# Optimization experiments

Measured on AMD Instinct MI355X. Metric: run time of the kernel, lower is better.

The kernel has to match this reference:

```python
import math
import jax, jax.numpy as jnp
import numpy as np

B, NQ, NKV, D, H = 32, 512, 512, 1024, 8
DH = D // H              # 128
N_COLS = 512             # n + 1
D_COL = math.ceil(2 * math.log2(N_COLS))  # 18


def setup_inputs() -> dict:
    key = jax.random.key(0)
    ks = jax.random.split(key, 8)
    s = 0.02
    return {
        "x_q": jax.random.normal(ks[0], (B, NQ, D), jnp.float32),
        "x_kv": jax.random.normal(ks[1], (B, NKV, D), jnp.float32),
        # sym_weight=True => W_tail is W_head (shared)
        "W_head_w": jax.random.normal(ks[2], (D, D), jnp.float32) * s,
        "W_head_b": jnp.zeros((D,), jnp.float32),
        "W_v_w": jax.random.normal(ks[3], (D, D), jnp.float32) * s,
        "W_v_b": jnp.zeros((D,), jnp.float32),
        "W_out_w": jax.random.normal(ks[4], (D, D), jnp.float32) * s,
        "W_out_b": jnp.zeros((D,), jnp.float32),
        "rel_emb": jnp.ones((H, DH), jnp.float32),
        "col_head": jax.random.normal(ks[5], (H, N_COLS, D_COL), jnp.float32) * 0.2,
        "col_tail": jax.random.normal(ks[6], (H, N_COLS, D_COL), jnp.float32) * 0.2,
    }


def _heads(x, W, b, h, dh):
    # Linear then split heads: [B, n, d] -> [B, H, n, dh]
    B_, n, _ = x.shape
    y = x @ W.T + b
    return y.reshape(B_, n, h, dh).transpose(0, 2, 1, 3)


def reference(x_q, x_kv, W_head_w, W_head_b, W_v_w, W_v_b,
              W_out_w, W_out_b, rel_emb, col_head, col_tail):
    Bb, nq, d = x_q.shape
    nkv = x_kv.shape[1]
    h, dh = rel_emb.shape

    f_head = _heads(x_q, W_head_w, W_head_b, h, dh) * rel_emb[None, :, None, :]
    f_tail = _heads(x_kv, W_head_w, W_head_b, h, dh) * rel_emb[None, :, None, :]  # W_tail = W_head (sym_weight)
    f_v = _heads(x_kv, W_v_w, W_v_b, h, dh)

    # content score: [B, H, nq, nkv]
    weight_score = jnp.einsum('bhqd,bhkd->bhqk', f_head, f_tail) / math.sqrt(dh)

    # learned column topology: [H, n_cols, n_cols]
    adj_logits = jnp.einsum('hqc,hkc->hqk', col_head, col_tail)
    eye = jnp.eye(adj_logits.shape[-1], dtype=bool)  # nsi: zero diagonal before softmax
    adj_logits = jnp.where(eye[None], 0.0, adj_logits)
    adj = jax.nn.softmax(adj_logits, axis=-1)[:, :nq, :nkv]

    adj_mask = (1.0 - adj) * -10000.0
    fr_graph = jax.nn.softmax(weight_score + adj_mask[None], axis=-1)

    x = jnp.einsum('bhqk,bhkd->bhqd', fr_graph, f_v)
    x = x.transpose(0, 2, 1, 3).reshape(Bb, nq, h * dh)
    x = x @ W_out_w.T + W_out_b
    return (x, fr_graph.reshape(Bb * h, nq, nkv))
```

## Files before the change

### kernel.cpp

```cpp
#include <hip/hip_runtime.h>

typedef __attribute__((ext_vector_type(8))) __bf16 bf8;
typedef __attribute__((ext_vector_type(4))) __bf16 bf4;
typedef __attribute__((ext_vector_type(4))) float f32x4;

#define DEVI static __device__ __forceinline__

DEVI void gload_lds16(const void* g, void* l) {
  __builtin_amdgcn_global_load_lds(
      (const __attribute__((address_space(1))) unsigned int*)g,
      (__attribute__((address_space(3))) unsigned int*)l, 16, 0, 0);
}

__global__ __launch_bounds__(256) void cvt_kernel(const float* __restrict__ in,
                                                  __bf16* __restrict__ out, int n4) {
  int stride = gridDim.x * blockDim.x;
  for (int i = blockIdx.x * blockDim.x + threadIdx.x; i < n4; i += stride) {
    f32x4 v = reinterpret_cast<const f32x4*>(in)[i];
    bf4 o;
    o[0] = (__bf16)v[0]; o[1] = (__bf16)v[1]; o[2] = (__bf16)v[2]; o[3] = (__bf16)v[3];
    reinterpret_cast<bf4*>(out)[i] = o;
  }
}

template <int MODE>
__global__ __launch_bounds__(256) void gemm_proj(
    const __bf16* __restrict__ A, const __bf16* __restrict__ Bw,
    const float* __restrict__ bias, const float* __restrict__ rel,
    __bf16* __restrict__ obf, float* __restrict__ of32) {
  __shared__ alignas(16) __bf16 As[128 * 64];
  __shared__ alignas(16) __bf16 Bs[128 * 64];
  const int tid = threadIdx.x;
  const int lane = tid & 63;
  const int wave = tid >> 6;
  const int wr = wave >> 1, wc = wave & 1;
  const int lr = lane & 15, lk = (lane >> 4) * 8;

  f32x4 acc[4][4];
#pragma unroll
  for (int i = 0; i < 4; ++i)
#pragma unroll
    for (int j = 0; j < 4; ++j)
#pragma unroll
      for (int e = 0; e < 4; ++e) acc[i][j][e] = 0.f;

  const __bf16* Ab = A + (size_t)blockIdx.y * 128 * 1024;
  const __bf16* Bb = Bw + (size_t)blockIdx.x * 128 * 1024;
  const int sr = tid >> 3;
  const int sc = (tid & 7) * 8;

  for (int kt = 0; kt < 1024; kt += 64) {
#pragma unroll
    for (int i = 0; i < 4; ++i) {
      gload_lds16(Ab + (size_t)(sr + i * 32) * 1024 + kt + sc, As + tid * 8 + i * 2048);
      gload_lds16(Bb + (size_t)(sr + i * 32) * 1024 + kt + sc, Bs + tid * 8 + i * 2048);
    }
    __syncthreads();
#pragma unroll
    for (int kk = 0; kk < 64; kk += 32) {
      bf8 a[4], b[4];
#pragma unroll
      for (int mi = 0; mi < 4; ++mi)
        a[mi] = *reinterpret_cast<const bf8*>(&As[(wr * 64 + mi * 16 + lr) * 64 + kk + lk]);
#pragma unroll
      for (int ni = 0; ni < 4; ++ni)
        b[ni] = *reinterpret_cast<const bf8*>(&Bs[(wc * 64 + ni * 16 + lr) * 64 + kk + lk]);
#pragma unroll
      for (int mi = 0; mi < 4; ++mi)
#pragma unroll
        for (int ni = 0; ni < 4; ++ni)
          acc[mi][ni] = __builtin_amdgcn_mfma_f32_16x16x32_bf16(a[mi], b[ni], acc[mi][ni], 0, 0, 0);
    }
    __syncthreads();
  }

  const int mBase = blockIdx.y * 128 + wr * 64;
  const int nBase = blockIdx.x * 128 + wc * 64;
#pragma unroll
  for (int mi = 0; mi < 4; ++mi) {
#pragma unroll
    for (int ni = 0; ni < 4; ++ni) {
      const int n = nBase + ni * 16 + lr;
#pragma unroll
      for (int r = 0; r < 4; ++r) {
        const int m = mBase + mi * 16 + (lane >> 4) * 4 + r;
        float v = acc[mi][ni][r] + bias[n];
        if (MODE == 0) v *= rel[n];
        if (MODE == 2) {
          of32[(size_t)m * 1024 + n] = v;
        } else if (MODE == 0) {
          size_t idx = ((size_t)((m >> 9) * 8 + (n >> 7))) * 65536 +
                       (size_t)(m & 511) * 128 + (n & 127);
          obf[idx] = (__bf16)v;
        } else {
          size_t idx = ((size_t)((m >> 9) * 8 + (n >> 7))) * 65536 +
                       (size_t)(n & 127) * 512 + (m & 511);
          obf[idx] = (__bf16)v;
        }
      }
    }
  }
}

__global__ __launch_bounds__(256) void adj_kernel(const float* __restrict__ ch_all,
                                                  const float* __restrict__ ct_all,
                                                  float* __restrict__ adjs) {
  const int wave = threadIdx.x >> 6, lane = threadIdx.x & 63;
  const int row = blockIdx.x * 4 + wave;
  const int h = row >> 9, i = row & 511;
  float ch[18];
  const float* chp = ch_all + ((size_t)h * 512 + i) * 18;
#pragma unroll
  for (int t = 0; t < 18; ++t) ch[t] = chp[t];
  float e[8];
  float m = -1e30f;
#pragma unroll
  for (int jj = 0; jj < 8; ++jj) {
    const int j = jj * 64 + lane;
    const float* ctp = ct_all + ((size_t)h * 512 + j) * 18;
    float d = 0.f;
#pragma unroll
    for (int t = 0; t < 18; ++t) d += ch[t] * ctp[t];
    if (j == i) d = 0.f;
    e[jj] = d;
    m = fmaxf(m, d);
  }
#pragma unroll
  for (int off = 32; off >= 1; off >>= 1) m = fmaxf(m, __shfl_xor(m, off));
  float s = 0.f;
#pragma unroll
  for (int jj = 0; jj < 8; ++jj) { e[jj] = __expf(e[jj] - m); s += e[jj]; }
#pragma unroll
  for (int off = 32; off >= 1; off >>= 1) s += __shfl_xor(s, off);
  const float inv = 10000.f / s;
  float* op = adjs + (size_t)h * 262144 + (size_t)i * 512;
#pragma unroll
  for (int jj = 0; jj < 8; ++jj) op[jj * 64 + lane] = e[jj] * inv;
}

__global__ __launch_bounds__(256) void fused_attn_kernel(
    const __bf16* __restrict__ fh, const __bf16* __restrict__ ft,
    const __bf16* __restrict__ fvT, const float* __restrict__ adjs,
    float* fr, __bf16* __restrict__ ctx) {
  __shared__ alignas(16) __bf16 Bt[128 * 128];
  const int tid = threadIdx.x;
  const int l = tid & 63, w = tid >> 6;
  const int qt = blockIdx.x;
  const int bh = blockIdx.y;
  const int b = bh >> 3, h = bh & 7;
  const int wrow = qt * 64 + w * 16;
  const int lr = l & 15, lk = (l >> 4) * 8;

  bf8 afr[4];
  {
    const __bf16* ap = fh + (size_t)bh * 65536 + (size_t)(wrow + lr) * 128 + lk;
#pragma unroll
    for (int kk4 = 0; kk4 < 4; ++kk4)
      afr[kk4] = *reinterpret_cast<const bf8*>(ap + kk4 * 32);
  }

  f32x4 acc[32];
#pragma unroll
  for (int n = 0; n < 32; ++n)
#pragma unroll
    for (int e = 0; e < 4; ++e) acc[n][e] = 0.f;

  const __bf16* ftb = ft + (size_t)bh * 65536;
#pragma unroll
  for (int kt = 0; kt < 4; ++kt) {
    __syncthreads();
#pragma unroll
    for (int i = 0; i < 8; ++i)
      gload_lds16(ftb + (size_t)(kt * 128 + i * 16 + (tid >> 4)) * 128 + (tid & 15) * 8,
                  Bt + i * 2048 + tid * 8);
    __syncthreads();
#pragma unroll
    for (int kk4 = 0; kk4 < 4; ++kk4) {
      bf8 bfr[8];
#pragma unroll
      for (int n2 = 0; n2 < 8; ++n2)
        bfr[n2] = *reinterpret_cast<const bf8*>(&Bt[(n2 * 16 + lr) * 128 + kk4 * 32 + lk]);
#pragma unroll
      for (int n2 = 0; n2 < 8; ++n2)
        acc[kt * 8 + n2] =
            __builtin_amdgcn_mfma_f32_16x16x32_bf16(afr[kk4], bfr[n2], acc[kt * 8 + n2], 0, 0, 0);
    }
  }

  const float scale = 0.08838834764831845f;
  const float* adjp = adjs + (size_t)h * 262144;
  float mrow[4] = {-1e30f, -1e30f, -1e30f, -1e30f};
#pragma unroll
  for (int n = 0; n < 32; ++n) {
    const int col = n * 16 + lr;
#pragma unroll
    for (int r = 0; r < 4; ++r) {
      const int q = wrow + (l >> 4) * 4 + r;
      float v = acc[n][r] * scale + adjp[(size_t)q * 512 + col];
      acc[n][r] = v;
      mrow[r] = fmaxf(mrow[r], v);
    }
  }
#pragma unroll
  for (int r = 0; r < 4; ++r)
#pragma unroll
    for (int off = 1; off <= 8; off <<= 1) mrow[r] = fmaxf(mrow[r], __shfl_xor(mrow[r], off));
  float srow[4] = {0.f, 0.f, 0.f, 0.f};
#pragma unroll
  for (int n = 0; n < 32; ++n)
#pragma unroll
    for (int r = 0; r < 4; ++r) {
      float e = __expf(acc[n][r] - mrow[r]);
      acc[n][r] = e;
      srow[r] += e;
    }
#pragma unroll
  for (int r = 0; r < 4; ++r)
#pragma unroll
    for (int off = 1; off <= 8; off <<= 1) srow[r] += __shfl_xor(srow[r], off);
  float inv[4];
#pragma unroll
  for (int r = 0; r < 4; ++r) inv[r] = 1.f / srow[r];

  float* frb = fr + (size_t)bh * 262144;
#pragma unroll
  for (int n = 0; n < 32; ++n) {
    const int col = n * 16 + lr;
#pragma unroll
    for (int r = 0; r < 4; ++r) {
      const int q = wrow + (l >> 4) * 4 + r;
      acc[n][r] *= inv[r];
      frb[(size_t)q * 512 + col] = acc[n][r];
    }
  }

  f32x4 acc2[8];
#pragma unroll
  for (int n2 = 0; n2 < 8; ++n2)
#pragma unroll
    for (int e = 0; e < 4; ++e) acc2[n2][e] = 0.f;

  const __bf16* fvb = fvT + (size_t)bh * 65536;
  const float* frr = fr + (size_t)bh * 262144 + (size_t)(wrow + lr) * 512;
  asm volatile("s_waitcnt vmcnt(0)" ::: "memory");
#pragma unroll
  for (int kt = 0; kt < 4; ++kt) {
    __syncthreads();
#pragma unroll
    for (int i = 0; i < 8; ++i)
      gload_lds16(fvb + (size_t)(i * 16 + (tid >> 4)) * 512 + kt * 128 + (tid & 15) * 8,
                  Bt + i * 2048 + tid * 8);
    __syncthreads();
#pragma unroll
    for (int kk4 = 0; kk4 < 4; ++kk4) {
      const float* src = frr + kt * 128 + kk4 * 32 + lk;
      f32x4 x0 = *reinterpret_cast<const f32x4*>(src);
      f32x4 x1 = *reinterpret_cast<const f32x4*>(src + 4);
      bf8 av;
      av[0] = (__bf16)x0[0]; av[1] = (__bf16)x0[1];
      av[2] = (__bf16)x0[2]; av[3] = (__bf16)x0[3];
      av[4] = (__bf16)x1[0]; av[5] = (__bf16)x1[1];
      av[6] = (__bf16)x1[2]; av[7] = (__bf16)x1[3];
      bf8 bfr[8];
#pragma unroll
      for (int n2 = 0; n2 < 8; ++n2)
        bfr[n2] = *reinterpret_cast<const bf8*>(&Bt[(n2 * 16 + lr) * 128 + kk4 * 32 + lk]);
#pragma unroll
      for (int n2 = 0; n2 < 8; ++n2)
        acc2[n2] = __builtin_amdgcn_mfma_f32_16x16x32_bf16(av, bfr[n2], acc2[n2], 0, 0, 0);
    }
  }
#pragma unroll
  for (int n2 = 0; n2 < 8; ++n2) {
    const int c = n2 * 16 + lr;
#pragma unroll
    for (int r = 0; r < 4; ++r) {
      const int q = wrow + (l >> 4) * 4 + r;
      ctx[(size_t)(b * 512 + q) * 1024 + h * 128 + c] = (__bf16)acc2[n2][r];
    }
  }
}

extern "C" void kernel_launch(void* const* d_in, const int* in_sizes, int n_in,
                              void* d_out, int out_size, void* d_ws, size_t ws_size,
                              hipStream_t stream) {
  const float* x_q  = (const float*)d_in[0];
  const float* x_kv = (const float*)d_in[1];
  const float* Wh   = (const float*)d_in[2];
  const float* bh   = (const float*)d_in[3];
  const float* Wv   = (const float*)d_in[4];
  const float* bv   = (const float*)d_in[5];
  const float* Wo   = (const float*)d_in[6];
  const float* bo   = (const float*)d_in[7];
  const float* rel  = (const float*)d_in[8];
  const float* colh = (const float*)d_in[9];
  const float* colt = (const float*)d_in[10];

  float* out = (float*)d_out;
  float* fr  = out + 16777216;

  __bf16* xq_bf  = (__bf16*)d_ws;
  __bf16* xkv_bf = xq_bf + 16777216;
  __bf16* Wh_bf  = xkv_bf + 16777216;
  __bf16* Wv_bf  = Wh_bf + 1048576;
  __bf16* Wo_bf  = Wv_bf + 1048576;
  __bf16* fhead  = Wo_bf + 1048576;
  __bf16* ftail  = fhead + 16777216;
  __bf16* fvT    = ftail + 16777216;
  float*  adjs   = (float*)(fvT + 16777216);
  __bf16* ctx    = (__bf16*)(adjs + 2097152);

  cvt_kernel<<<4096, 256, 0, stream>>>(x_q, xq_bf, 4194304);
  cvt_kernel<<<4096, 256, 0, stream>>>(x_kv, xkv_bf, 4194304);
  cvt_kernel<<<1024, 256, 0, stream>>>(Wh, Wh_bf, 262144);
  cvt_kernel<<<1024, 256, 0, stream>>>(Wv, Wv_bf, 262144);
  cvt_kernel<<<1024, 256, 0, stream>>>(Wo, Wo_bf, 262144);

  dim3 gp(8, 128);
  gemm_proj<0><<<gp, 256, 0, stream>>>(xq_bf, Wh_bf, bh, rel, fhead, nullptr);
  gemm_proj<0><<<gp, 256, 0, stream>>>(xkv_bf, Wh_bf, bh, rel, ftail, nullptr);
  gemm_proj<1><<<gp, 256, 0, stream>>>(xkv_bf, Wv_bf, bv, nullptr, fvT, nullptr);

  adj_kernel<<<1024, 256, 0, stream>>>(colh, colt, adjs);

  fused_attn_kernel<<<dim3(8, 256), 256, 0, stream>>>(fhead, ftail, fvT, adjs, fr, ctx);

  gemm_proj<2><<<gp, 256, 0, stream>>>(ctx, Wo_bf, bo, nullptr, nullptr, out);
}
```

Measured before the change: 900.0 us.

## Feed attention probabilities to PV matmul through LDS and swizzle shared tiles

The fused attention kernel now converts the normalized probabilities to bf16 in a per-wave LDS buffer for the PV matmul, instead of writing fr to global memory and reading it back. It also XOR-swizzles the K/V LDS tiles to avoid bank conflicts, prefetches V tiles while fr is stored, and stores the adjacency bias transposed so it can be read as float4 vectors. Grid orders are swapped for the GEMMs and the attention kernel to change block scheduling and cache reuse, and the attention kernel gets an occupancy hint of 3 blocks. The extra LDS and the occupancy hint could add register pressure or spills.

Result: no change. 895.5 us (-0.5%).

```diff
diff --git a/kernel.cpp b/kernel.cpp
--- a/kernel.cpp
+++ b/kernel.cpp
@@ -35,6 +35,7 @@
   const int wave = tid >> 6;
   const int wr = wave >> 1, wc = wave & 1;
   const int lr = lane & 15, lk = (lane >> 4) * 8;
+  const int bm = blockIdx.x, bn = blockIdx.y;
 
   f32x4 acc[4][4];
 #pragma unroll
@@ -44,8 +45,8 @@
 #pragma unroll
       for (int e = 0; e < 4; ++e) acc[i][j][e] = 0.f;
 
-  const __bf16* Ab = A + (size_t)blockIdx.y * 128 * 1024;
-  const __bf16* Bb = Bw + (size_t)blockIdx.x * 128 * 1024;
+  const __bf16* Ab = A + (size_t)bm * 128 * 1024;
+  const __bf16* Bb = Bw + (size_t)bn * 128 * 1024;
   const int sr = tid >> 3;
   const int sc = (tid & 7) * 8;
 
@@ -74,8 +75,8 @@
     __syncthreads();
   }
 
-  const int mBase = blockIdx.y * 128 + wr * 64;
-  const int nBase = blockIdx.x * 128 + wc * 64;
+  const int mBase = bm * 128 + wr * 64;
+  const int nBase = bn * 128 + wc * 64;
 #pragma unroll
   for (int mi = 0; mi < 4; ++mi) {
 #pragma unroll
@@ -104,7 +105,7 @@
 
 __global__ __launch_bounds__(256) void adj_kernel(const float* __restrict__ ch_all,
                                                   const float* __restrict__ ct_all,
-                                                  float* __restrict__ adjs) {
+                                                  float* __restrict__ adjT) {
   const int wave = threadIdx.x >> 6, lane = threadIdx.x & 63;
   const int row = blockIdx.x * 4 + wave;
   const int h = row >> 9, i = row & 511;
@@ -133,27 +134,32 @@
 #pragma unroll
   for (int off = 32; off >= 1; off >>= 1) s += __shfl_xor(s, off);
   const float inv = 10000.f / s;
-  float* op = adjs + (size_t)h * 262144 + (size_t)i * 512;
-#pragma unroll
-  for (int jj = 0; jj < 8; ++jj) op[jj * 64 + lane] = e[jj] * inv;
-}
-
-__global__ __launch_bounds__(256) void fused_attn_kernel(
+  float* op = adjT + (size_t)h * 262144 + i;
+#pragma unroll
+  for (int jj = 0; jj < 8; ++jj) op[(size_t)(jj * 64 + lane) * 512] = e[jj] * inv;
+}
+
+__global__ __launch_bounds__(256, 3) void fused_attn_kernel(
     const __bf16* __restrict__ fh, const __bf16* __restrict__ ft,
-    const __bf16* __restrict__ fvT, const float* __restrict__ adjs,
-    float* fr, __bf16* __restrict__ ctx) {
+    const __bf16* __restrict__ fvT, const float* __restrict__ adjT,
+    float* __restrict__ fr, __bf16* __restrict__ ctx) {
   __shared__ alignas(16) __bf16 Bt[128 * 128];
+  __shared__ alignas(16) __bf16 Pl[4][16 * 128];
   const int tid = threadIdx.x;
   const int l = tid & 63, w = tid >> 6;
-  const int qt = blockIdx.x;
-  const int bh = blockIdx.y;
+  const int bh = blockIdx.x;
+  const int qt = blockIdx.y;
   const int b = bh >> 3, h = bh & 7;
   const int wrow = qt * 64 + w * 16;
-  const int lr = l & 15, lk = (l >> 4) * 8;
+  const int lr = l & 15;
+  const int khi = l >> 4;
+
+  const int srow = tid >> 4;
+  const int scc = (tid & 15) ^ (srow & 7);
 
   bf8 afr[4];
   {
-    const __bf16* ap = fh + (size_t)bh * 65536 + (size_t)(wrow + lr) * 128 + lk;
+    const __bf16* ap = fh + (size_t)bh * 65536 + (size_t)(wrow + lr) * 128 + khi * 8;
 #pragma unroll
     for (int kk4 = 0; kk4 < 4; ++kk4)
       afr[kk4] = *reinterpret_cast<const bf8*>(ap + kk4 * 32);
@@ -168,10 +174,9 @@
   const __bf16* ftb = ft + (size_t)bh * 65536;
 #pragma unroll
   for (int kt = 0; kt < 4; ++kt) {
-    __syncthreads();
 #pragma unroll
     for (int i = 0; i < 8; ++i)
-      gload_lds16(ftb + (size_t)(kt * 128 + i * 16 + (tid >> 4)) * 128 + (tid & 15) * 8,
+      gload_lds16(ftb + (size_t)(kt * 128 + i * 16 + srow) * 128 + scc * 8,
                   Bt + i * 2048 + tid * 8);
     __syncthreads();
 #pragma unroll
@@ -179,24 +184,26 @@
       bf8 bfr[8];
 #pragma unroll
       for (int n2 = 0; n2 < 8; ++n2)
-        bfr[n2] = *reinterpret_cast<const bf8*>(&Bt[(n2 * 16 + lr) * 128 + kk4 * 32 + lk]);
+        bfr[n2] = *reinterpret_cast<const bf8*>(
+            &Bt[(n2 * 16 + lr) * 128 + ((kk4 * 4 + khi) ^ (lr & 7)) * 8]);
 #pragma unroll
       for (int n2 = 0; n2 < 8; ++n2)
         acc[kt * 8 + n2] =
             __builtin_amdgcn_mfma_f32_16x16x32_bf16(afr[kk4], bfr[n2], acc[kt * 8 + n2], 0, 0, 0);
     }
+    __syncthreads();
   }
 
   const float scale = 0.08838834764831845f;
-  const float* adjp = adjs + (size_t)h * 262144;
+  const float* adjTp = adjT + (size_t)h * 262144;
   float mrow[4] = {-1e30f, -1e30f, -1e30f, -1e30f};
 #pragma unroll
   for (int n = 0; n < 32; ++n) {
     const int col = n * 16 + lr;
+    f32x4 av = *reinterpret_cast<const f32x4*>(adjTp + (size_t)col * 512 + wrow + khi * 4);
 #pragma unroll
     for (int r = 0; r < 4; ++r) {
-      const int q = wrow + (l >> 4) * 4 + r;
-      float v = acc[n][r] * scale + adjp[(size_t)q * 512 + col];
+      float v = acc[n][r] * scale + av[r];
       acc[n][r] = v;
       mrow[r] = fmaxf(mrow[r], v);
     }
@@ -205,32 +212,40 @@
   for (int r = 0; r < 4; ++r)
 #pragma unroll
     for (int off = 1; off <= 8; off <<= 1) mrow[r] = fmaxf(mrow[r], __shfl_xor(mrow[r], off));
-  float srow[4] = {0.f, 0.f, 0.f, 0.f};
+  float srw[4] = {0.f, 0.f, 0.f, 0.f};
 #pragma unroll
   for (int n = 0; n < 32; ++n)
 #pragma unroll
     for (int r = 0; r < 4; ++r) {
       float e = __expf(acc[n][r] - mrow[r]);
       acc[n][r] = e;
-      srow[r] += e;
+      srw[r] += e;
     }
 #pragma unroll
   for (int r = 0; r < 4; ++r)
 #pragma unroll
-    for (int off = 1; off <= 8; off <<= 1) srow[r] += __shfl_xor(srow[r], off);
+    for (int off = 1; off <= 8; off <<= 1) srw[r] += __shfl_xor(srw[r], off);
   float inv[4];
 #pragma unroll
-  for (int r = 0; r < 4; ++r) inv[r] = 1.f / srow[r];
-
-  float* frb = fr + (size_t)bh * 262144;
-#pragma unroll
-  for (int n = 0; n < 32; ++n) {
-    const int col = n * 16 + lr;
-#pragma unroll
-    for (int r = 0; r < 4; ++r) {
-      const int q = wrow + (l >> 4) * 4 + r;
-      acc[n][r] *= inv[r];
-      frb[(size_t)q * 512 + col] = acc[n][r];
+  for (int r = 0; r < 4; ++r) inv[r] = 1.f / srw[r];
+#pragma unroll
+  for (int n = 0; n < 32; ++n)
+#pragma unroll
+    for (int r = 0; r < 4; ++r) acc[n][r] *= inv[r];
+
+  const __bf16* fvb = fvT + (size_t)bh * 65536;
+#pragma unroll
+  for (int i = 0; i < 8; ++i)
+    gload_lds16(fvb + (size_t)(i * 16 + srow) * 512 + scc * 8, Bt + i * 2048 + tid * 8);
+
+  {
+    float* frb = fr + (size_t)bh * 262144;
+#pragma unroll
+    for (int n = 0; n < 32; ++n) {
+      const int col = n * 16 + lr;
+#pragma unroll
+      for (int r = 0; r < 4; ++r)
+        frb[(size_t)(wrow + khi * 4 + r) * 512 + col] = acc[n][r];
     }
   }
 
@@ -240,42 +255,49 @@
 #pragma unroll
     for (int e = 0; e < 4; ++e) acc2[n2][e] = 0.f;
 
-  const __bf16* fvb = fvT + (size_t)bh * 65536;
-  const float* frr = fr + (size_t)bh * 262144 + (size_t)(wrow + lr) * 512;
-  asm volatile("s_waitcnt vmcnt(0)" ::: "memory");
+  __bf16* Pw = &Pl[w][0];
 #pragma unroll
   for (int kt = 0; kt < 4; ++kt) {
-    __syncthreads();
-#pragma unroll
-    for (int i = 0; i < 8; ++i)
-      gload_lds16(fvb + (size_t)(i * 16 + (tid >> 4)) * 512 + kt * 128 + (tid & 15) * 8,
-                  Bt + i * 2048 + tid * 8);
+#pragma unroll
+    for (int n2 = 0; n2 < 8; ++n2) {
+      const int colc = n2 * 2 + (lr >> 3);
+      const int cl = lr & 7;
+#pragma unroll
+      for (int r = 0; r < 4; ++r) {
+        const int q = khi * 4 + r;
+        Pw[q * 128 + ((colc ^ (q & 7)) * 8) + cl] = (__bf16)acc[kt * 8 + n2][r];
+      }
+    }
     __syncthreads();
 #pragma unroll
     for (int kk4 = 0; kk4 < 4; ++kk4) {
-      const float* src = frr + kt * 128 + kk4 * 32 + lk;
-      f32x4 x0 = *reinterpret_cast<const f32x4*>(src);
-      f32x4 x1 = *reinterpret_cast<const f32x4*>(src + 4);
-      bf8 av;
-      av[0] = (__bf16)x0[0]; av[1] = (__bf16)x0[1];
-      av[2] = (__bf16)x0[2]; av[3] = (__bf16)x0[3];
-      av[4] = (__bf16)x1[0]; av[5] = (__bf16)x1[1];
-      av[6] = (__bf16)x1[2]; av[7] = (__bf16)x1[3];
+      bf8 pa = *reinterpret_cast<const bf8*>(
+          &Pw[lr * 128 + ((kk4 * 4 + khi) ^ (lr & 7)) * 8]);
       bf8 bfr[8];
 #pragma unroll
       for (int n2 = 0; n2 < 8; ++n2)
-        bfr[n2] = *reinterpret_cast<const bf8*>(&Bt[(n2 * 16 + lr) * 128 + kk4 * 32 + lk]);
+        bfr[n2] = *reinterpret_cast<const bf8*>(
+            &Bt[(n2 * 16 + lr) * 128 + ((kk4 * 4 + khi) ^ (lr & 7)) * 8]);
 #pragma unroll
       for (int n2 = 0; n2 < 8; ++n2)
-        acc2[n2] = __builtin_amdgcn_mfma_f32_16x16x32_bf16(av, bfr[n2], acc2[n2], 0, 0, 0);
-    }
-  }
+        acc2[n2] = __builtin_amdgcn_mfma_f32_16x16x32_bf16(pa, bfr[n2], acc2[n2], 0, 0, 0);
+    }
+    __syncthreads();
+    if (kt < 3) {
+      const int ktn = kt + 1;
+#pragma unroll
+      for (int i = 0; i < 8; ++i)
+        gload_lds16(fvb + (size_t)(i * 16 + srow) * 512 + ktn * 128 + scc * 8,
+                    Bt + i * 2048 + tid * 8);
+    }
+  }
+
 #pragma unroll
   for (int n2 = 0; n2 < 8; ++n2) {
     const int c = n2 * 16 + lr;
 #pragma unroll
     for (int r = 0; r < 4; ++r) {
-      const int q = wrow + (l >> 4) * 4 + r;
+      const int q = wrow + khi * 4 + r;
       ctx[(size_t)(b * 512 + q) * 1024 + h * 128 + c] = (__bf16)acc2[n2][r];
     }
   }
@@ -307,8 +329,8 @@
   __bf16* fhead  = Wo_bf + 1048576;
   __bf16* ftail  = fhead + 16777216;
   __bf16* fvT    = ftail + 16777216;
-  float*  adjs   = (float*)(fvT + 16777216);
-  __bf16* ctx    = (__bf16*)(adjs + 2097152);
+  float*  adjT   = (float*)(fvT + 16777216);
+  __bf16* ctx    = (__bf16*)(adjT + 2097152);
 
   cvt_kernel<<<4096, 256, 0, stream>>>(x_q, xq_bf, 4194304);
   cvt_kernel<<<4096, 256, 0, stream>>>(x_kv, xkv_bf, 4194304);
@@ -316,14 +338,14 @@
   cvt_kernel<<<1024, 256, 0, stream>>>(Wv, Wv_bf, 262144);
   cvt_kernel<<<1024, 256, 0, stream>>>(Wo, Wo_bf, 262144);
 
-  dim3 gp(8, 128);
+  dim3 gp(128, 8);
   gemm_proj<0><<<gp, 256, 0, stream>>>(xq_bf, Wh_bf, bh, rel, fhead, nullptr);
   gemm_proj<0><<<gp, 256, 0, stream>>>(xkv_bf, Wh_bf, bh, rel, ftail, nullptr);
   gemm_proj<1><<<gp, 256, 0, stream>>>(xkv_bf, Wv_bf, bv, nullptr, fvT, nullptr);
 
-  adj_kernel<<<1024, 256, 0, stream>>>(colh, colt, adjs);
-
-  fused_attn_kernel<<<dim3(8, 256), 256, 0, stream>>>(fhead, ftail, fvT, adjs, fr, ctx);
+  adj_kernel<<<1024, 256, 0, stream>>>(colh, colt, adjT);
+
+  fused_attn_kernel<<<dim3(256, 8), 256, 0, stream>>>(fhead, ftail, fvT, adjT, fr, ctx);
 
   gemm_proj<2><<<gp, 256, 0, stream>>>(ctx, Wo_bf, bo, nullptr, nullptr, out);
 }
```
